# Performance work log

Hardware: AMD Instinct MI355X
Metric: run time of the kernel (lower is better)

## Reference

```python
import jax, jax.numpy as jnp
import numpy as np

B, F_DIM, C, M = 16, 64, 64, 512
OUT_CH = 32
DT = 1.0


def setup_inputs() -> dict:
    key = jax.random.key(0)
    ks = jax.random.split(key, 8)
    x = jax.random.normal(ks[0], (B, F_DIM, C, M), dtype=jnp.float32)
    A = jax.random.uniform(ks[1], (B, M, C, C), dtype=jnp.float32)
    phys_prior = jax.random.normal(ks[2], (B, C, M), dtype=jnp.float32)
    kappa = jnp.array(0.1, dtype=jnp.float32)
    alpha = jnp.array(0.05, dtype=jnp.float32)
    # r_phi MLP: Linear(1,16) -> ELU -> Linear(16,1)
    w1 = jax.random.normal(ks[3], (16, 1), dtype=jnp.float32) * 1.0
    b1 = jnp.zeros((16,), dtype=jnp.float32)
    w2 = jax.random.normal(ks[4], (1, 16), dtype=jnp.float32) * 0.25
    b2 = jnp.zeros((1,), dtype=jnp.float32)
    # 1x1 Conv2d(1, OUT_CH): weight (OUT_CH,1,1,1) -> flatten to (OUT_CH,)
    pw = jax.random.normal(ks[5], (OUT_CH,), dtype=jnp.float32)
    pb = jnp.zeros((OUT_CH,), dtype=jnp.float32)
    return {"x": x, "A": A, "phys_prior": phys_prior, "kappa": kappa,
            "alpha": alpha, "w1": w1, "b1": b1, "w2": w2, "b2": b2,
            "pw": pw, "pb": pb}


def reference(x, A, phys_prior, kappa, alpha, w1, b1, w2, b2, pw, pb):
    # x: (B,F,C,M), A: (B,M,C,C), phys_prior: (B,C,M)
    s = x.mean(axis=1)                      # (B,C,M)
    deg = A.sum(axis=-1)                    # (B,M,C)
    sT = jnp.transpose(s, (0, 2, 1))        # (B,M,C)
    # torch einsum 'bmcd,bmcn->bmdn' with n=1 contracts over c: (A^T s)
    As = jnp.einsum('bmcd,bmc->bmd', A, sT)  # (B,M,C)
    Ls = jnp.transpose(deg * sT - As, (0, 2, 1))  # (B,C,M)
    k = jax.nn.softplus(kappa)
    # tiny MLP on per-(b,c) mean over M
    r_in = s.mean(axis=-1, keepdims=True)   # (B,C,1)
    h = jax.nn.elu(r_in @ w1.T + b1)        # (B,C,16)
    r = h @ w2.T + b2                       # (B,C,1), broadcasts over M
    phys_corr = alpha * phys_prior          # (B,C,M)
    s_new = s - DT * k * Ls + DT * (r + phys_corr)  # (B,C,M)
    # 1x1 conv over (B,1,C,M): pointwise scale+bias per output channel
    corr = s_new[:, None, :, :] * pw[None, :, None, None] + pb[None, :, None, None]
    return corr  # (B,OUT_CH,C,M)
```

## Files before the change

### kernel.cpp

```cpp
#include <hip/hip_runtime.h>
#include <math.h>

#define B_  16
#define F_  64
#define C_  64
#define M_  512
#define OC_ 32

__global__ __launch_bounds__(128, 6) void k1_mean(
    const float* __restrict__ x,
    float* __restrict__ s_out, float* __restrict__ rpart)
{
    const int gid = blockIdx.x;
    const int q   = gid & 3;
    const int bc  = gid >> 2;
    const int b   = bc >> 6;
    const int c   = bc & 63;
    const int t   = threadIdx.x;
    const int tf  = t >> 5;
    const int tm  = t & 31;
    const int m4  = (q << 5) + tm;

    const size_t rowbase = ((size_t)b * F_ * C_ + c) * M_;
    float ax = 0.f, ay = 0.f, az = 0.f, aw = 0.f;
    #pragma unroll 8
    for (int j = 0; j < 16; ++j) {
        const int f = (tf << 4) + j;
        const float4 v = ((const float4*)(x + rowbase + (size_t)f * C_ * M_))[m4];
        ax += v.x; ay += v.y; az += v.z; aw += v.w;
    }

    __shared__ float4 red[4][32];
    red[tf][tm] = make_float4(ax, ay, az, aw);
    __syncthreads();

    if (tf == 0) {
        const float4 r1 = red[1][tm], r2 = red[2][tm], r3 = red[3][tm];
        const float inv_f = 1.0f / (float)F_;
        float4 sv;
        sv.x = (ax + r1.x + r2.x + r3.x) * inv_f;
        sv.y = (ay + r1.y + r2.y + r3.y) * inv_f;
        sv.z = (az + r1.z + r2.z + r3.z) * inv_f;
        sv.w = (aw + r1.w + r2.w + r3.w) * inv_f;
        ((float4*)(s_out + (size_t)bc * M_))[m4] = sv;

        float p = sv.x + sv.y + sv.z + sv.w;
        #pragma unroll
        for (int off = 16; off > 0; off >>= 1) p += __shfl_xor(p, off);
        if (t == 0) rpart[gid] = p;
    }
}

__global__ __launch_bounds__(256) void k2_laplace(
    const float* __restrict__ A, const float* __restrict__ phys,
    const float* __restrict__ kappa_p, const float* __restrict__ alpha_p,
    const float* __restrict__ s_in, const float* __restrict__ rpart,
    const float* __restrict__ w1, const float* __restrict__ b1,
    const float* __restrict__ w2, const float* __restrict__ b2,
    float* __restrict__ snew)
{
    __shared__ float Al[C_ * 65];
    __shared__ float sl[C_];
    __shared__ float redD[4 * C_];
    __shared__ float redA[4 * C_];

    const int bm = blockIdx.x;
    const int b  = bm >> 9;
    const int m  = bm & 511;
    const int t  = threadIdx.x;
    const int c  = t & 63;
    const int q  = t >> 6;

    float r = 0.f;
    if (t < 64) {
        const float4 rp = ((const float4*)rpart)[b * C_ + t];
        const float rin = (rp.x + rp.y + rp.z + rp.w) * (1.0f / (float)M_);
        r = b2[0];
        #pragma unroll
        for (int j = 0; j < 16; ++j) {
            float h = rin * w1[j] + b1[j];
            h = (h > 0.f) ? h : (expf(h) - 1.f);
            r += h * w2[j];
        }
        sl[t] = s_in[((size_t)b * C_ + t) * M_ + m];
    }

    const float4* Ap = (const float4*)(A + (size_t)bm * (C_ * C_));
    #pragma unroll
    for (int i = 0; i < 4; ++i) {
        const int idx = t + i * 256;
        const float4 v = Ap[idx];
        const int row = idx >> 4;
        const int col = (idx & 15) << 2;
        float* dst = &Al[row * 65 + col];
        dst[0] = v.x; dst[1] = v.y; dst[2] = v.z; dst[3] = v.w;
    }
    __syncthreads();

    float dpart = 0.f, apart = 0.f;
    const int j0 = q << 4;
    #pragma unroll
    for (int j = 0; j < 16; ++j) {
        dpart += Al[c * 65 + (j0 + j)];
        apart += Al[(j0 + j) * 65 + c] * sl[j0 + j];
    }
    redD[(q << 6) + c] = dpart;
    redA[(q << 6) + c] = apart;
    __syncthreads();

    if (t < 64) {
        const float deg = redD[t] + redD[64 + t] + redD[128 + t] + redD[192 + t];
        const float As  = redA[t] + redA[64 + t] + redA[128 + t] + redA[192 + t];
        const float sval = sl[t];
        const float k    = log1pf(expf(kappa_p[0]));
        const float Ls   = deg * sval - As;
        const float val  = sval - k * Ls
                         + (r + alpha_p[0] * phys[((size_t)b * C_ + t) * M_ + m]);
        snew[((size_t)b * C_ + t) * M_ + m] = val;
    }
}

__global__ __launch_bounds__(256) void k3_expand(
    const float* __restrict__ snew,
    const float* __restrict__ pw, const float* __restrict__ pb,
    float* __restrict__ out)
{
    const int n4 = (B_ * OC_ * C_ * M_) / 4;
    for (int i = blockIdx.x * blockDim.x + threadIdx.x; i < n4;
         i += gridDim.x * blockDim.x) {
        const int m4 = i & 127;
        const int c  = (i >> 7) & 63;
        const int o  = (i >> 13) & 31;
        const int b  = i >> 18;
        const float4 v = ((const float4*)snew)[(((b << 6) + c) << 7) + m4];
        const float w  = pw[o];
        const float bb = pb[o];
        float4 r;
        r.x = v.x * w + bb; r.y = v.y * w + bb;
        r.z = v.z * w + bb; r.w = v.w * w + bb;
        ((float4*)out)[i] = r;
    }
}

extern "C" void kernel_launch(void* const* d_in, const int* in_sizes, int n_in,
                              void* d_out, int out_size, void* d_ws, size_t ws_size,
                              hipStream_t stream)
{
    const float* x     = (const float*)d_in[0];
    const float* A     = (const float*)d_in[1];
    const float* phys  = (const float*)d_in[2];
    const float* kappa = (const float*)d_in[3];
    const float* alpha = (const float*)d_in[4];
    const float* w1    = (const float*)d_in[5];
    const float* b1    = (const float*)d_in[6];
    const float* w2    = (const float*)d_in[7];
    const float* b2    = (const float*)d_in[8];
    const float* pw    = (const float*)d_in[9];
    const float* pb    = (const float*)d_in[10];
    float* out = (float*)d_out;

    float* ws    = (float*)d_ws;
    float* s     = ws;
    float* snew  = ws + (size_t)B_ * C_ * M_;
    float* rpart = ws + (size_t)2 * B_ * C_ * M_;

    k1_mean<<<B_ * C_ * 4, 128, 0, stream>>>(x, s, rpart);
    k2_laplace<<<B_ * M_, 256, 0, stream>>>(A, phys, kappa, alpha, s, rpart,
                                            w1, b1, w2, b2, snew);
    k3_expand<<<2048, 256, 0, stream>>>(snew, pw, pb, out);
}
```

Measured before the change: 74.89 us.

## Fuse Laplacian and channel expansion kernels with double-buffered A tiles per m-window

Merges the Laplacian update and the 1x1-conv expansion into one kernel. Each block handles 16 consecutive m positions and streams the A matrices through a double-buffered shared-memory tile, prefetching the next slice into registers. The s_new tile stays in shared memory and is written directly as 32 output channels, removing the snew round trip and a launch. The trade-off is a grid cut from 8192 to 512 blocks and more shared memory per block, which lowers parallelism for streaming the 32 MB A array.

```diff
diff --git a/kernel.cpp b/kernel.cpp
--- a/kernel.cpp
+++ b/kernel.cpp
@@ -6,6 +6,7 @@
 #define C_  64
 #define M_  512
 #define OC_ 32
+#define W_  16
 
 __global__ __launch_bounds__(128, 6) void k1_mean(
     const float* __restrict__ x,
@@ -51,25 +52,40 @@
     }
 }
 
-__global__ __launch_bounds__(256) void k2_laplace(
+__global__ __launch_bounds__(256) void k2_fused(
     const float* __restrict__ A, const float* __restrict__ phys,
     const float* __restrict__ kappa_p, const float* __restrict__ alpha_p,
     const float* __restrict__ s_in, const float* __restrict__ rpart,
     const float* __restrict__ w1, const float* __restrict__ b1,
     const float* __restrict__ w2, const float* __restrict__ b2,
-    float* __restrict__ snew)
+    const float* __restrict__ pw, const float* __restrict__ pb,
+    float* __restrict__ out)
 {
-    __shared__ float Al[C_ * 65];
-    __shared__ float sl[C_];
-    __shared__ float redD[4 * C_];
-    __shared__ float redA[4 * C_];
-
-    const int bm = blockIdx.x;
-    const int b  = bm >> 9;
-    const int m  = bm & 511;
-    const int t  = threadIdx.x;
-    const int c  = t & 63;
-    const int q  = t >> 6;
+    __shared__ float Al[2][C_ * 65];
+    __shared__ float s_l[C_][W_ + 1];
+    __shared__ float ph_l[C_][W_ + 1];
+    __shared__ float sn_l[C_][W_ + 1];
+    __shared__ float redD[4][C_];
+    __shared__ float redA[4][C_];
+
+    const int blk = blockIdx.x;
+    const int b   = blk >> 5;
+    const int m0  = (blk & 31) << 4;
+    const int t   = threadIdx.x;
+    const int c   = t & 63;
+    const int q   = t >> 6;
+
+    {
+        const int rr = t >> 2;
+        const int mq = (t & 3) << 2;
+        const size_t g = ((size_t)b * C_ + rr) * M_ + m0 + mq;
+        const float4 sv = *(const float4*)(s_in + g);
+        const float4 pv = *(const float4*)(phys + g);
+        s_l[rr][mq + 0] = sv.x; s_l[rr][mq + 1] = sv.y;
+        s_l[rr][mq + 2] = sv.z; s_l[rr][mq + 3] = sv.w;
+        ph_l[rr][mq + 0] = pv.x; ph_l[rr][mq + 1] = pv.y;
+        ph_l[rr][mq + 2] = pv.z; ph_l[rr][mq + 3] = pv.w;
+    }
 
     float r = 0.f;
     if (t < 64) {
@@ -82,63 +98,84 @@
             h = (h > 0.f) ? h : (expf(h) - 1.f);
             r += h * w2[j];
         }
-        sl[t] = s_in[((size_t)b * C_ + t) * M_ + m];
-    }
-
-    const float4* Ap = (const float4*)(A + (size_t)bm * (C_ * C_));
+    }
+
+    const float* Abase = A + ((size_t)b * M_ + m0) * (C_ * C_);
+    float4 pre[4];
+    #pragma unroll
+    for (int i = 0; i < 4; ++i) pre[i] = ((const float4*)Abase)[t + i * 256];
     #pragma unroll
     for (int i = 0; i < 4; ++i) {
         const int idx = t + i * 256;
-        const float4 v = Ap[idx];
         const int row = idx >> 4;
         const int col = (idx & 15) << 2;
-        float* dst = &Al[row * 65 + col];
-        dst[0] = v.x; dst[1] = v.y; dst[2] = v.z; dst[3] = v.w;
+        float* dst = &Al[0][row * 65 + col];
+        dst[0] = pre[i].x; dst[1] = pre[i].y; dst[2] = pre[i].z; dst[3] = pre[i].w;
     }
     __syncthreads();
 
-    float dpart = 0.f, apart = 0.f;
-    const int j0 = q << 4;
-    #pragma unroll
-    for (int j = 0; j < 16; ++j) {
-        dpart += Al[c * 65 + (j0 + j)];
-        apart += Al[(j0 + j) * 65 + c] * sl[j0 + j];
-    }
-    redD[(q << 6) + c] = dpart;
-    redA[(q << 6) + c] = apart;
-    __syncthreads();
-
-    if (t < 64) {
-        const float deg = redD[t] + redD[64 + t] + redD[128 + t] + redD[192 + t];
-        const float As  = redA[t] + redA[64 + t] + redA[128 + t] + redA[192 + t];
-        const float sval = sl[t];
-        const float k    = log1pf(expf(kappa_p[0]));
-        const float Ls   = deg * sval - As;
-        const float val  = sval - k * Ls
-                         + (r + alpha_p[0] * phys[((size_t)b * C_ + t) * M_ + m]);
-        snew[((size_t)b * C_ + t) * M_ + m] = val;
-    }
-}
-
-__global__ __launch_bounds__(256) void k3_expand(
-    const float* __restrict__ snew,
-    const float* __restrict__ pw, const float* __restrict__ pb,
-    float* __restrict__ out)
-{
-    const int n4 = (B_ * OC_ * C_ * M_) / 4;
-    for (int i = blockIdx.x * blockDim.x + threadIdx.x; i < n4;
-         i += gridDim.x * blockDim.x) {
-        const int m4 = i & 127;
-        const int c  = (i >> 7) & 63;
-        const int o  = (i >> 13) & 31;
-        const int b  = i >> 18;
-        const float4 v = ((const float4*)snew)[(((b << 6) + c) << 7) + m4];
-        const float w  = pw[o];
-        const float bb = pb[o];
-        float4 r;
-        r.x = v.x * w + bb; r.y = v.y * w + bb;
-        r.z = v.z * w + bb; r.w = v.w * w + bb;
-        ((float4*)out)[i] = r;
+    const float k  = log1pf(expf(kappa_p[0]));
+    const float al = alpha_p[0];
+
+    for (int mi = 0; mi < W_; ++mi) {
+        const int cur = mi & 1;
+
+        if (mi < W_ - 1) {
+            const float4* Ap = (const float4*)(Abase + (size_t)(mi + 1) * (C_ * C_));
+            #pragma unroll
+            for (int i = 0; i < 4; ++i) pre[i] = Ap[t + i * 256];
+        }
+
+        float dpart = 0.f, apart = 0.f;
+        const int j0 = q << 4;
+        #pragma unroll
+        for (int j = 0; j < 16; ++j) {
+            dpart += Al[cur][c * 65 + (j0 + j)];
+            apart += Al[cur][(j0 + j) * 65 + c] * s_l[j0 + j][mi];
+        }
+        redD[q][c] = dpart;
+        redA[q][c] = apart;
+        __syncthreads();
+
+        if (t < 64) {
+            const float deg  = redD[0][t] + redD[1][t] + redD[2][t] + redD[3][t];
+            const float As   = redA[0][t] + redA[1][t] + redA[2][t] + redA[3][t];
+            const float sval = s_l[t][mi];
+            const float Ls   = deg * sval - As;
+            sn_l[t][mi] = sval - k * Ls + (r + al * ph_l[t][mi]);
+        }
+
+        if (mi < W_ - 1) {
+            #pragma unroll
+            for (int i = 0; i < 4; ++i) {
+                const int idx = t + i * 256;
+                const int row = idx >> 4;
+                const int col = (idx & 15) << 2;
+                float* dst = &Al[cur ^ 1][row * 65 + col];
+                dst[0] = pre[i].x; dst[1] = pre[i].y;
+                dst[2] = pre[i].z; dst[3] = pre[i].w;
+            }
+        }
+        __syncthreads();
+    }
+
+    {
+        const int rr = t >> 2;
+        const int mq = (t & 3) << 2;
+        const float v0 = sn_l[rr][mq + 0];
+        const float v1 = sn_l[rr][mq + 1];
+        const float v2 = sn_l[rr][mq + 2];
+        const float v3 = sn_l[rr][mq + 3];
+        const size_t obase = (((size_t)b * OC_) * C_ + rr) * M_ + m0 + mq;
+        #pragma unroll 4
+        for (int o = 0; o < OC_; ++o) {
+            const float w  = pw[o];
+            const float bb = pb[o];
+            float4 ov;
+            ov.x = v0 * w + bb; ov.y = v1 * w + bb;
+            ov.z = v2 * w + bb; ov.w = v3 * w + bb;
+            *(float4*)(out + obase + (size_t)o * (C_ * M_)) = ov;
+        }
     }
 }
 
@@ -161,11 +198,9 @@
 
     float* ws    = (float*)d_ws;
     float* s     = ws;
-    float* snew  = ws + (size_t)B_ * C_ * M_;
-    float* rpart = ws + (size_t)2 * B_ * C_ * M_;
+    float* rpart = ws + (size_t)B_ * C_ * M_;
 
     k1_mean<<<B_ * C_ * 4, 128, 0, stream>>>(x, s, rpart);
-    k2_laplace<<<B_ * M_, 256, 0, stream>>>(A, phys, kappa, alpha, s, rpart,
-                                            w1, b1, w2, b2, snew);
-    k3_expand<<<2048, 256, 0, stream>>>(snew, pw, pb, out);
+    k2_fused<<<B_ * (M_ / W_), 256, 0, stream>>>(A, phys, kappa, alpha, s, rpart,
+                                                 w1, b1, w2, b2, pw, pb, out);
 }
```

Measured after the change: 90.80 us. 21.2% more time.

## Restructure Laplacian kernel: one wavefront per m, register A tiles, shuffle reductions

Applied to the files above, without the earlier changes.

The Laplacian kernel now handles four m values per block, one 64-lane wavefront each. Each wavefront loads its 64x64 A tile directly into registers, with no LDS staging, and computes row sums and the A^T s product with cross-lane shuffle butterfly reductions. The s, phys and MLP terms are staged once per block and the results are written as coalesced float4 vectors. The aim is to remove LDS traffic, block syncs and scattered scalar global accesses, at the cost of heavier register pressure (64 float4 registers per lane).

```diff
diff --git a/kernel.cpp b/kernel.cpp
--- a/kernel.cpp
+++ b/kernel.cpp
@@ -51,7 +51,7 @@
     }
 }
 
-__global__ __launch_bounds__(256) void k2_laplace(
+__global__ __launch_bounds__(256, 4) void k2_laplace(
     const float* __restrict__ A, const float* __restrict__ phys,
     const float* __restrict__ kappa_p, const float* __restrict__ alpha_p,
     const float* __restrict__ s_in, const float* __restrict__ rpart,
@@ -59,64 +59,109 @@
     const float* __restrict__ w2, const float* __restrict__ b2,
     float* __restrict__ snew)
 {
-    __shared__ float Al[C_ * 65];
-    __shared__ float sl[C_];
-    __shared__ float redD[4 * C_];
-    __shared__ float redA[4 * C_];
-
-    const int bm = blockIdx.x;
-    const int b  = bm >> 9;
-    const int m  = bm & 511;
-    const int t  = threadIdx.x;
-    const int c  = t & 63;
-    const int q  = t >> 6;
-
-    float r = 0.f;
+    __shared__ float s_l[C_ * 5];
+    __shared__ float ph_l[C_ * 5];
+    __shared__ float sn_l[C_ * 5];
+    __shared__ float r_l[C_];
+
+    const int blk = blockIdx.x;
+    const int b   = blk >> 7;
+    const int m0  = (blk & 127) << 2;
+    const int t   = threadIdx.x;
+
     if (t < 64) {
-        const float4 rp = ((const float4*)rpart)[b * C_ + t];
+        const float4 sv = *(const float4*)(s_in + ((size_t)(b * C_ + t)) * M_ + m0);
+        s_l[t*5+0] = sv.x; s_l[t*5+1] = sv.y; s_l[t*5+2] = sv.z; s_l[t*5+3] = sv.w;
+    } else if (t < 128) {
+        const int tt = t - 64;
+        const float4 pv = *(const float4*)(phys + ((size_t)(b * C_ + tt)) * M_ + m0);
+        ph_l[tt*5+0] = pv.x; ph_l[tt*5+1] = pv.y; ph_l[tt*5+2] = pv.z; ph_l[tt*5+3] = pv.w;
+    } else if (t < 192) {
+        const int tt = t - 128;
+        const float4 rp = ((const float4*)rpart)[b * C_ + tt];
         const float rin = (rp.x + rp.y + rp.z + rp.w) * (1.0f / (float)M_);
-        r = b2[0];
+        float r = b2[0];
         #pragma unroll
         for (int j = 0; j < 16; ++j) {
-            float h = rin * w1[j] + b1[j];
-            h = (h > 0.f) ? h : (expf(h) - 1.f);
-            r += h * w2[j];
+            float hh = rin * w1[j] + b1[j];
+            hh = (hh > 0.f) ? hh : (expf(hh) - 1.f);
+            r += hh * w2[j];
         }
-        sl[t] = s_in[((size_t)b * C_ + t) * M_ + m];
-    }
-
-    const float4* Ap = (const float4*)(A + (size_t)bm * (C_ * C_));
-    #pragma unroll
-    for (int i = 0; i < 4; ++i) {
-        const int idx = t + i * 256;
-        const float4 v = Ap[idx];
-        const int row = idx >> 4;
-        const int col = (idx & 15) << 2;
-        float* dst = &Al[row * 65 + col];
-        dst[0] = v.x; dst[1] = v.y; dst[2] = v.z; dst[3] = v.w;
+        r_l[tt] = r;
     }
     __syncthreads();
 
-    float dpart = 0.f, apart = 0.f;
-    const int j0 = q << 4;
+    const int w = t >> 6;
+    const int l = t & 63;
+    const int g = l >> 4;
+    const int h = l & 15;
+
+    const float4* Ap = (const float4*)(A + ((size_t)(b * M_ + m0 + w)) * (C_ * C_));
+    float4 v[16];
+    #pragma unroll
+    for (int j = 0; j < 16; ++j) v[j] = Ap[j * 64 + l];
+
+    float d[16];
+    float a0 = 0.f, a1 = 0.f, a2 = 0.f, a3 = 0.f;
     #pragma unroll
     for (int j = 0; j < 16; ++j) {
-        dpart += Al[c * 65 + (j0 + j)];
-        apart += Al[(j0 + j) * 65 + c] * sl[j0 + j];
-    }
-    redD[(q << 6) + c] = dpart;
-    redA[(q << 6) + c] = apart;
+        const float sr = s_l[(4*j + g) * 5 + w];
+        d[j] = v[j].x + v[j].y + v[j].z + v[j].w;
+        a0 += sr * v[j].x; a1 += sr * v[j].y;
+        a2 += sr * v[j].z; a3 += sr * v[j].w;
+    }
+
+    float e[8];
+    #pragma unroll
+    for (int jj = 0; jj < 8; ++jj) {
+        const float sd = (h & 8) ? d[jj] : d[jj + 8];
+        const float rv = __shfl_xor(sd, 8);
+        e[jj] = ((h & 8) ? d[jj + 8] : d[jj]) + rv;
+    }
+    float f2[4];
+    #pragma unroll
+    for (int jj = 0; jj < 4; ++jj) {
+        const float sd = (h & 4) ? e[jj] : e[jj + 4];
+        const float rv = __shfl_xor(sd, 4);
+        f2[jj] = ((h & 4) ? e[jj + 4] : e[jj]) + rv;
+    }
+    float g2[2];
+    #pragma unroll
+    for (int jj = 0; jj < 2; ++jj) {
+        const float sd = (h & 2) ? f2[jj] : f2[jj + 2];
+        const float rv = __shfl_xor(sd, 2);
+        g2[jj] = ((h & 2) ? f2[jj + 2] : f2[jj]) + rv;
+    }
+    float deg;
+    {
+        const float sd = (h & 1) ? g2[0] : g2[1];
+        const float rv = __shfl_xor(sd, 1);
+        deg = ((h & 1) ? g2[1] : g2[0]) + rv;
+    }
+
+    const float send0 = (g & 1) ? a0 : a1;
+    const float send1 = (g & 1) ? a2 : a3;
+    const float r0 = __shfl_xor(send0, 16);
+    const float r1 = __shfl_xor(send1, 16);
+    const float b0v = ((g & 1) ? a1 : a0) + r0;
+    const float b1v = ((g & 1) ? a3 : a2) + r1;
+    const float send2 = (g & 2) ? b0v : b1v;
+    const float r2 = __shfl_xor(send2, 32);
+    const float Asv = ((g & 2) ? b1v : b0v) + r2;
+
+    const float kk = log1pf(expf(kappa_p[0]));
+    const float al = alpha_p[0];
+    const int   i  = 4 * h + g;
+    const float sval = s_l[i * 5 + w];
+    const float Ls   = deg * sval - Asv;
+    sn_l[i * 5 + w]  = sval - kk * Ls + (r_l[i] + al * ph_l[i * 5 + w]);
     __syncthreads();
 
     if (t < 64) {
-        const float deg = redD[t] + redD[64 + t] + redD[128 + t] + redD[192 + t];
-        const float As  = redA[t] + redA[64 + t] + redA[128 + t] + redA[192 + t];
-        const float sval = sl[t];
-        const float k    = log1pf(expf(kappa_p[0]));
-        const float Ls   = deg * sval - As;
-        const float val  = sval - k * Ls
-                         + (r + alpha_p[0] * phys[((size_t)b * C_ + t) * M_ + m]);
-        snew[((size_t)b * C_ + t) * M_ + m] = val;
+        float4 ov;
+        ov.x = sn_l[t*5+0]; ov.y = sn_l[t*5+1];
+        ov.z = sn_l[t*5+2]; ov.w = sn_l[t*5+3];
+        *(float4*)(snew + ((size_t)(b * C_ + t)) * M_ + m0) = ov;
     }
 }
 
@@ -165,7 +210,7 @@
     float* rpart = ws + (size_t)2 * B_ * C_ * M_;
 
     k1_mean<<<B_ * C_ * 4, 128, 0, stream>>>(x, s, rpart);
-    k2_laplace<<<B_ * M_, 256, 0, stream>>>(A, phys, kappa, alpha, s, rpart,
-                                            w1, b1, w2, b2, snew);
+    k2_laplace<<<B_ * (M_ / 4), 256, 0, stream>>>(A, phys, kappa, alpha, s, rpart,
+                                                  w1, b1, w2, b2, snew);
     k3_expand<<<2048, 256, 0, stream>>>(snew, pw, pb, out);
 }
```

Measured after the change: 77.55 us. 3.5% more time.
